# Kernel optimization log

Measured on AMD Instinct MI355X. Metric: run time of the kernel, lower is better.

## Reference

```python
import jax, jax.numpy as jnp
import numpy as np

N = 100_000      # nodes
E = 600_000      # edges (before self-loops)
F_IN = 128       # in_channels
H0, H1 = 64, 128 # hidden_channels
D = 512          # FLAGS.D
G = 512          # number of graphs in batch
OUT = 1          # FLAGS.out_dim


def _lin(key, fan_in, fan_out):
    k1, k2 = jax.random.split(key)
    s = 1.0 / np.sqrt(fan_in)
    return (jax.random.uniform(k1, (fan_in, fan_out), jnp.float32, -s, s),
            jax.random.uniform(k2, (fan_out,), jnp.float32, -s, s))


def setup_inputs() -> dict:
    key = jax.random.key(0)
    ks = jax.random.split(key, 12)
    x = jax.random.normal(ks[0], (N, F_IN), jnp.float32)
    src = jax.random.randint(ks[1], (E,), 0, N, jnp.int32)
    dst = jax.random.randint(ks[2], (E,), 0, N, jnp.int32)
    batch = jnp.sort(jax.random.randint(ks[3], (N,), 0, G, jnp.int32))
    Wc0, bc0 = _lin(ks[4], F_IN, H0)   # GCNConv 1
    Wc1, bc1 = _lin(ks[5], H0, H1)     # GCNConv 2
    Wf, bf = _lin(ks[6], H1, D)        # first_MLP: Linear(128, D)
    Wh0, bh0 = _lin(ks[7], D, D // 2)  # MLP head hidden layers
    Wh1, bh1 = _lin(ks[8], D // 2, D // 4)
    Wh2, bh2 = _lin(ks[9], D // 4, D // 8)
    Wo, bo = _lin(ks[10], D // 8, OUT) # MLP head output
    return dict(x=x, src=src, dst=dst, batch=batch,
                Wc0=Wc0, bc0=bc0, Wc1=Wc1, bc1=bc1, Wf=Wf, bf=bf,
                Wh0=Wh0, bh0=bh0, Wh1=Wh1, bh1=bh1, Wh2=Wh2, bh2=bh2,
                Wo=Wo, bo=bo)


def gcn_conv(x, src, dst, W, b):
    """PyG GCNConv: add self-loops, sym-normalized neighbor sum, then bias."""
    n = x.shape[0]
    loop = jnp.arange(n, dtype=src.dtype)
    s = jnp.concatenate([src, loop])
    d = jnp.concatenate([dst, loop])
    deg = jax.ops.segment_sum(jnp.ones(s.shape[0], x.dtype), d, num_segments=n)
    dinv = jnp.where(deg > 0, jax.lax.rsqrt(deg), 0.0)
    h = x @ W                                  # [n, out]
    coeff = (dinv[s] * dinv[d])[:, None]       # [e+n, 1]
    out = jax.ops.segment_sum(h[s] * coeff, d, num_segments=n)
    return out + b


def reference(x, src, dst, batch, Wc0, bc0, Wc1, bc1, Wf, bf,
              Wh0, bh0, Wh1, bh1, Wh2, bh2, Wo, bo):
    # two GCNConv layers + ReLU (dropout p=0.0 is a no-op)
    h = jax.nn.relu(gcn_conv(x, src, dst, Wc0, bc0))
    h = jax.nn.relu(gcn_conv(h, src, dst, Wc1, bc1))
    # global mean pool over graphs
    cnt = jax.ops.segment_sum(jnp.ones(h.shape[0], h.dtype), batch, num_segments=G)
    g = jax.ops.segment_sum(h, batch, num_segments=G) / jnp.maximum(cnt, 1.0)[:, None]
    # first_MLP (plain Linear) then MLP head with ReLU hidden layers
    e = g @ Wf + bf
    e = jax.nn.relu(e @ Wh0 + bh0)
    e = jax.nn.relu(e @ Wh1 + bh1)
    e = jax.nn.relu(e @ Wh2 + bh2)
    out = e @ Wo + bo
    return out
```

## Files before the change

### kernel.cpp

```cpp
#include <hip/hip_runtime.h>
#include <hip/hip_bf16.h>

#define NN   100000
#define NE   600000
#define FIN  128
#define H0   64
#define H1   128
#define NG   512
#define BM   64
#define XP   132
#define AP   68

__global__ void hist_kernel(const int* __restrict__ idx, int* __restrict__ cnt, int n)
{
    int i = blockIdx.x * blockDim.x + threadIdx.x;
    int stride = gridDim.x * blockDim.x;
    for (; i < n; i += stride) atomicAdd(&cnt[idx[i]], 1);
}

__global__ void batch_count_kernel(const int* __restrict__ batch,
                                   int* __restrict__ cnt, int n)
{
    const int g = blockIdx.x * blockDim.x + threadIdx.x;
    if (g >= NG) return;
    int lo = 0, hi = n;
    while (lo < hi) { const int m = (lo + hi) >> 1; if (batch[m] < g) lo = m + 1; else hi = m; }
    const int start = lo;
    lo = 0; hi = n;
    while (lo < hi) { const int m = (lo + hi) >> 1; if (batch[m] < g + 1) lo = m + 1; else hi = m; }
    cnt[g] = lo - start;
}

__global__ void dinv_kernel(const int* __restrict__ deg, float* __restrict__ dinv, int n)
{
    int i = blockIdx.x * blockDim.x + threadIdx.x;
    if (i < n) dinv[i] = 1.0f / sqrtf((float)(deg[i] + 1));
}

__global__ __launch_bounds__(256) void scan1_kernel(
    const int* __restrict__ deg, int* __restrict__ rp, int* __restrict__ bsum, int n)
{
    __shared__ int tmp[256];
    const int t = threadIdx.x;
    const int i = blockIdx.x * 256 + t;
    int v = (i < n) ? deg[i] : 0;
    tmp[t] = v;
    __syncthreads();
    #pragma unroll
    for (int off = 1; off < 256; off <<= 1) {
        int a = (t >= off) ? tmp[t - off] : 0;
        __syncthreads();
        tmp[t] += a;
        __syncthreads();
    }
    if (i < n) rp[i] = tmp[t] - v;
    if (t == 255) bsum[blockIdx.x] = tmp[255];
}

__global__ __launch_bounds__(512) void scan2_kernel(
    const int* __restrict__ bsum, int* __restrict__ boff, int nb)
{
    __shared__ int tmp[512];
    const int t = threadIdx.x;
    int v = (t < nb) ? bsum[t] : 0;
    tmp[t] = v;
    __syncthreads();
    #pragma unroll
    for (int off = 1; off < 512; off <<= 1) {
        int a = (t >= off) ? tmp[t - off] : 0;
        __syncthreads();
        tmp[t] += a;
        __syncthreads();
    }
    if (t < nb) boff[t] = tmp[t] - v;
}

__global__ __launch_bounds__(256) void scan3_kernel(
    int* __restrict__ rp, int* __restrict__ wcur, const int* __restrict__ boff, int n)
{
    const int i = blockIdx.x * 256 + threadIdx.x;
    if (i < n) {
        const int v = rp[i] + boff[blockIdx.x];
        rp[i] = v;
        wcur[i] = v;
    }
}

__global__ void fill_kernel(const int* __restrict__ src, const int* __restrict__ dst,
                            int* __restrict__ wcur, int* __restrict__ csr, int ne)
{
    int i = blockIdx.x * blockDim.x + threadIdx.x;
    const int stride = gridDim.x * blockDim.x;
    for (; i < ne; i += stride) {
        const int d = dst[i];
        const int p = atomicAdd(&wcur[d], 1);
        csr[p] = src[i];
    }
}

__global__ __launch_bounds__(256) void gemm1_kernel(
    const float* __restrict__ x, const float* __restrict__ W,
    const float* __restrict__ dinv, float* __restrict__ h0s, int n)
{
    __shared__ float Wl[FIN * H0];
    __shared__ float xs[BM * XP];
    const int t = threadIdx.x;
    for (int i = t; i < FIN * H0 / 4; i += 256)
        ((float4*)Wl)[i] = ((const float4*)W)[i];

    const int lane = t & 63;
    const int w    = t >> 6;
    const int rsub = lane >> 4;
    const int j0   = (lane & 15) * 4;
    const int wrow = w * 16 + rsub * 4;
    const int ntiles = (n + BM - 1) / BM;

    for (int tile = blockIdx.x; tile < ntiles; tile += gridDim.x) {
        const int row0  = tile * BM;
        const int nrows = min(BM, n - row0);
        __syncthreads();
        {
            const float4* xg = (const float4*)(x + (size_t)row0 * FIN);
            const int nf4 = nrows * (FIN / 4);
            for (int idx = t; idx < nf4; idx += 256) {
                const int r  = idx >> 5;
                const int c4 = idx & 31;
                *(float4*)&xs[r * XP + (c4 << 2)] = xg[idx];
            }
        }
        __syncthreads();

        float acc[4][4] = {};
        const float* xr = xs + wrow * XP;
        #pragma unroll 4
        for (int k = 0; k < FIN; k += 4) {
            const float4 w0 = *(const float4*)&Wl[(k + 0) * H0 + j0];
            const float4 w1 = *(const float4*)&Wl[(k + 1) * H0 + j0];
            const float4 w2 = *(const float4*)&Wl[(k + 2) * H0 + j0];
            const float4 w3 = *(const float4*)&Wl[(k + 3) * H0 + j0];
            #pragma unroll
            for (int r = 0; r < 4; ++r) {
                const float4 xv = *(const float4*)&xr[r * XP + k];
                acc[r][0] += xv.x * w0.x; acc[r][0] += xv.y * w1.x;
                acc[r][0] += xv.z * w2.x; acc[r][0] += xv.w * w3.x;
                acc[r][1] += xv.x * w0.y; acc[r][1] += xv.y * w1.y;
                acc[r][1] += xv.z * w2.y; acc[r][1] += xv.w * w3.y;
                acc[r][2] += xv.x * w0.z; acc[r][2] += xv.y * w1.z;
                acc[r][2] += xv.z * w2.z; acc[r][2] += xv.w * w3.z;
                acc[r][3] += xv.x * w0.w; acc[r][3] += xv.y * w1.w;
                acc[r][3] += xv.z * w2.w; acc[r][3] += xv.w * w3.w;
            }
        }
        #pragma unroll
        for (int r = 0; r < 4; ++r) {
            const int row = row0 + wrow + r;
            if (row < n) {
                const float dv = dinv[row];
                float4 o;
                o.x = acc[r][0] * dv; o.y = acc[r][1] * dv;
                o.z = acc[r][2] * dv; o.w = acc[r][3] * dv;
                *(float4*)&h0s[(size_t)row * H0 + j0] = o;
            }
        }
    }
}

template <int MODE>
__global__ __launch_bounds__(256) void gather_kernel(
    const float* __restrict__ hin, const int* __restrict__ rowptr,
    const int* __restrict__ deg, const int* __restrict__ csr,
    const float* __restrict__ dinv, const float* __restrict__ bias,
    float* __restrict__ hout, int n)
{
    const int lane = threadIdx.x & 63;
    int wid = (blockIdx.x * blockDim.x + threadIdx.x) >> 6;
    const int nw = (gridDim.x * blockDim.x) >> 6;
    for (int d = wid; d < n; d += nw) {
        const int r0  = rowptr[d];
        const int cnt = deg[d];
        float acc = hin[(size_t)d * H0 + lane];
        int k = 0;
        for (; k + 1 < cnt; k += 2) {
            const int s0 = csr[r0 + k];
            const int s1 = csr[r0 + k + 1];
            acc += hin[(size_t)s0 * H0 + lane];
            acc += hin[(size_t)s1 * H0 + lane];
        }
        if (k < cnt) acc += hin[(size_t)csr[r0 + k] * H0 + lane];
        const float dv = dinv[d];
        if (MODE == 0)
            hout[(size_t)d * H0 + lane] = fmaxf(acc * dv + bias[lane], 0.f) * dv;
        else
            hout[(size_t)d * H0 + lane] = acc * dv;
    }
}

__global__ __launch_bounds__(256) void gemm2_pool_kernel(
    const float* __restrict__ a , const float* __restrict__ W ,
    const float* __restrict__ bc1, const int* __restrict__ batch,
    float* __restrict__ gsum, int n)
{
    __shared__ float Wl[H0 * H1];
    __shared__ float as[BM * AP];
    __shared__ float red[4][H1];
    __shared__ int   bs[BM];
    const int t = threadIdx.x;
    for (int i = t; i < H0 * H1 / 4; i += 256)
        ((float4*)Wl)[i] = ((const float4*)W)[i];

    const int lane = t & 63;
    const int w    = t >> 6;
    const int rsub = lane >> 4;
    const int cA   = (lane & 15) * 4;
    const int cB   = cA + 64;
    const int wrow = w * 16 + rsub * 4;
    const float4 bA = *(const float4*)&bc1[cA];
    const float4 bB = *(const float4*)&bc1[cB];
    const int ntiles = (n + BM - 1) / BM;

    for (int tile = blockIdx.x; tile < ntiles; tile += gridDim.x) {
        const int row0  = tile * BM;
        const int nrows = min(BM, n - row0);
        __syncthreads();
        {
            const float4* ag = (const float4*)(a + (size_t)row0 * H0);
            const int nf4 = nrows * (H0 / 4);
            for (int idx = t; idx < nf4; idx += 256) {
                const int r  = idx >> 4;
                const int c4 = idx & 15;
                *(float4*)&as[r * AP + (c4 << 2)] = ag[idx];
            }
            if (t < nrows) bs[t] = batch[row0 + t];
        }
        __syncthreads();

        float acc[4][8] = {};
        const float* ar = as + wrow * AP;
        #pragma unroll 4
        for (int k = 0; k < H0; k += 4) {
            float4 wa[4], wb[4];
            #pragma unroll
            for (int kk = 0; kk < 4; ++kk) {
                wa[kk] = *(const float4*)&Wl[(k + kk) * H1 + cA];
                wb[kk] = *(const float4*)&Wl[(k + kk) * H1 + cB];
            }
            #pragma unroll
            for (int r = 0; r < 4; ++r) {
                const float4 xv = *(const float4*)&ar[r * AP + k];
                acc[r][0] += xv.x * wa[0].x; acc[r][0] += xv.y * wa[1].x;
                acc[r][0] += xv.z * wa[2].x; acc[r][0] += xv.w * wa[3].x;
                acc[r][1] += xv.x * wa[0].y; acc[r][1] += xv.y * wa[1].y;
                acc[r][1] += xv.z * wa[2].y; acc[r][1] += xv.w * wa[3].y;
                acc[r][2] += xv.x * wa[0].z; acc[r][2] += xv.y * wa[1].z;
                acc[r][2] += xv.z * wa[2].z; acc[r][2] += xv.w * wa[3].z;
                acc[r][3] += xv.x * wa[0].w; acc[r][3] += xv.y * wa[1].w;
                acc[r][3] += xv.z * wa[2].w; acc[r][3] += xv.w * wa[3].w;
                acc[r][4] += xv.x * wb[0].x; acc[r][4] += xv.y * wb[1].x;
                acc[r][4] += xv.z * wb[2].x; acc[r][4] += xv.w * wb[3].x;
                acc[r][5] += xv.x * wb[0].y; acc[r][5] += xv.y * wb[1].y;
                acc[r][5] += xv.z * wb[2].y; acc[r][5] += xv.w * wb[3].y;
                acc[r][6] += xv.x * wb[0].z; acc[r][6] += xv.y * wb[1].z;
                acc[r][6] += xv.z * wb[2].z; acc[r][6] += xv.w * wb[3].z;
                acc[r][7] += xv.x * wb[0].w; acc[r][7] += xv.y * wb[1].w;
                acc[r][7] += xv.z * wb[2].w; acc[r][7] += xv.w * wb[3].w;
            }
        }

        const float bv[8] = {bA.x, bA.y, bA.z, bA.w, bB.x, bB.y, bB.z, bB.w};
        const bool uni = (nrows == BM) && (bs[0] == bs[BM - 1]);
        if (uni) {
            float s[8];
            #pragma unroll
            for (int c = 0; c < 8; ++c) {
                s[c] = fmaxf(acc[0][c] + bv[c], 0.f) + fmaxf(acc[1][c] + bv[c], 0.f)
                     + fmaxf(acc[2][c] + bv[c], 0.f) + fmaxf(acc[3][c] + bv[c], 0.f);
                s[c] += __shfl_xor(s[c], 16);
                s[c] += __shfl_xor(s[c], 32);
            }
            if (rsub == 0) {
                #pragma unroll
                for (int c = 0; c < 4; ++c) red[w][cA + c] = s[c];
                #pragma unroll
                for (int c = 0; c < 4; ++c) red[w][cB + c] = s[c + 4];
            }
            __syncthreads();
            if (t < H1)
                atomicAdd(&gsum[(size_t)bs[0] * H1 + t],
                          red[0][t] + red[1][t] + red[2][t] + red[3][t]);
        } else {
            int gcur = -1; float run[8];
            #pragma unroll
            for (int r = 0; r < 4; ++r) {
                const int row = wrow + r;
                if (row < nrows) {
                    const int g = bs[row];
                    if (g != gcur) {
                        if (gcur >= 0) {
                            #pragma unroll
                            for (int c = 0; c < 4; ++c)
                                atomicAdd(&gsum[(size_t)gcur * H1 + cA + c], run[c]);
                            #pragma unroll
                            for (int c = 0; c < 4; ++c)
                                atomicAdd(&gsum[(size_t)gcur * H1 + cB + c], run[c + 4]);
                        }
                        gcur = g;
                        #pragma unroll
                        for (int c = 0; c < 8; ++c) run[c] = fmaxf(acc[r][c] + bv[c], 0.f);
                    } else {
                        #pragma unroll
                        for (int c = 0; c < 8; ++c) run[c] += fmaxf(acc[r][c] + bv[c], 0.f);
                    }
                }
            }
            if (gcur >= 0) {
                #pragma unroll
                for (int c = 0; c < 4; ++c)
                    atomicAdd(&gsum[(size_t)gcur * H1 + cA + c], run[c]);
                #pragma unroll
                for (int c = 0; c < 4; ++c)
                    atomicAdd(&gsum[(size_t)gcur * H1 + cB + c], run[c + 4]);
            }
        }
    }
}

__global__ __launch_bounds__(256) void mlp_kernel(
    const float* __restrict__ gsum, const int* __restrict__ cnt,
    const float* __restrict__ Wf,  const float* __restrict__ bf,
    const float* __restrict__ Wh0, const float* __restrict__ bh0,
    const float* __restrict__ Wh1, const float* __restrict__ bh1,
    const float* __restrict__ Wh2, const float* __restrict__ bh2,
    const float* __restrict__ Wo,  const float* __restrict__ bo,
    float* __restrict__ out)
{
    __shared__ float gm[128];
    __shared__ float e0[512];
    __shared__ float e1[256];
    __shared__ float e2[128];
    __shared__ float e3[64];
    const int gi = blockIdx.x;
    const int t  = threadIdx.x;

    if (t < 128) {
        const int c = cnt[gi];
        gm[t] = gsum[gi * 128 + t] * (1.0f / (float)max(c, 1));
    }
    __syncthreads();

    for (int jj = t; jj < 512; jj += 256) {
        float acc = bf[jj];
        for (int k = 0; k < 128; ++k) acc += gm[k] * Wf[k * 512 + jj];
        e0[jj] = acc;
    }
    __syncthreads();

    {
        float acc = bh0[t];
        for (int k = 0; k < 512; ++k) acc += e0[k] * Wh0[k * 256 + t];
        if (t < 256) e1[t] = fmaxf(acc, 0.f);
    }
    __syncthreads();

    if (t < 128) {
        float acc = bh1[t];
        for (int k = 0; k < 256; ++k) acc += e1[k] * Wh1[k * 128 + t];
        e2[t] = fmaxf(acc, 0.f);
    }
    __syncthreads();

    if (t < 64) {
        float acc = bh2[t];
        for (int k = 0; k < 128; ++k) acc += e2[k] * Wh2[k * 64 + t];
        e3[t] = fmaxf(acc, 0.f);
    }
    __syncthreads();

    if (t < 64) {
        float p = e3[t] * Wo[t];
        #pragma unroll
        for (int off = 32; off > 0; off >>= 1) p += __shfl_down(p, off);
        if (t == 0) out[gi] = p + bo[0];
    }
}

extern "C" void kernel_launch(void* const* d_in, const int* in_sizes, int n_in,
                              void* d_out, int out_size, void* d_ws, size_t ws_size,
                              hipStream_t stream)
{
    const float* x    = (const float*)d_in[0];
    const int*   src  = (const int*)  d_in[1];
    const int*   dst  = (const int*)  d_in[2];
    const int*   batch= (const int*)  d_in[3];
    const float* Wc0  = (const float*)d_in[4];
    const float* bc0  = (const float*)d_in[5];
    const float* Wc1  = (const float*)d_in[6];
    const float* bc1  = (const float*)d_in[7];
    const float* Wf   = (const float*)d_in[8];
    const float* bf   = (const float*)d_in[9];
    const float* Wh0  = (const float*)d_in[10];
    const float* bh0  = (const float*)d_in[11];
    const float* Wh1  = (const float*)d_in[12];
    const float* bh1  = (const float*)d_in[13];
    const float* Wh2  = (const float*)d_in[14];
    const float* bh2  = (const float*)d_in[15];
    const float* Wo   = (const float*)d_in[16];
    const float* bo   = (const float*)d_in[17];
    float* out = (float*)d_out;

    const int n = NN, ne = NE;
    const int nblk = (n + 255) / 256;
    const int ntiles = (n + BM - 1) / BM;

    char* ws = (char*)d_ws;
    size_t off = 0;
    auto alloc = [&](size_t bytes) {
        void* p = ws + off;
        off = (off + bytes + 255) & ~(size_t)255;
        return p;
    };
    int*   deg    = (int*)  alloc((size_t)n * 4);
    float* dinv   = (float*)alloc((size_t)n * 4);
    int*   rowptr = (int*)  alloc((size_t)n * 4);
    int*   wcur   = (int*)  alloc((size_t)n * 4);
    int*   bsum   = (int*)  alloc(512 * 4);
    int*   boff   = (int*)  alloc(512 * 4);
    int*   csr    = (int*)  alloc((size_t)ne * 4);
    float* h0s    = (float*)alloc((size_t)n * H0 * 4);
    float* h1s    = (float*)alloc((size_t)n * H0 * 4);
    float* agg1   = (float*)alloc((size_t)n * H0 * 4);
    float* gsum   = (float*)alloc((size_t)NG * H1 * 4);
    int*   cnt    = (int*)  alloc((size_t)NG * 4);

    hipMemsetAsync(deg,  0, (size_t)n * 4, stream);
    hipMemsetAsync(gsum, 0, (size_t)NG * H1 * 4, stream);

    hist_kernel<<<1024, 256, 0, stream>>>(dst, deg, ne);
    batch_count_kernel<<<2, 256, 0, stream>>>(batch, cnt, n);
    dinv_kernel<<<nblk, 256, 0, stream>>>(deg, dinv, n);

    scan1_kernel<<<nblk, 256, 0, stream>>>(deg, rowptr, bsum, n);
    scan2_kernel<<<1, 512, 0, stream>>>(bsum, boff, nblk);
    scan3_kernel<<<nblk, 256, 0, stream>>>(rowptr, wcur, boff, n);
    fill_kernel<<<1024, 256, 0, stream>>>(src, dst, wcur, csr, ne);

    gemm1_kernel<<<ntiles, 256, 0, stream>>>(x, Wc0, dinv, h0s, n);
    gather_kernel<0><<<4096, 256, 0, stream>>>(h0s, rowptr, deg, csr, dinv, bc0, h1s, n);

    gather_kernel<1><<<4096, 256, 0, stream>>>(h1s, rowptr, deg, csr, dinv, bc0, agg1, n);
    gemm2_pool_kernel<<<ntiles, 256, 0, stream>>>(agg1, Wc1, bc1, batch, gsum, n);

    mlp_kernel<<<NG, 256, 0, stream>>>(gsum, cnt, Wf, bf, Wh0, bh0,
                                       Wh1, bh1, Wh2, bh2, Wo, bo, out);
}
```

Measured before the change: 389.1 us.

## Read GEMM weights from global/L1 instead of LDS; wave-cooperative CSR index loads in gather

Both GEMM kernels stop staging the weight matrix in shared memory and read it directly from global memory, relying on cache. This frees LDS and adds a launch-bounds occupancy hint of 4 blocks. The gather kernel now has the wave load up to 64 neighbor indices in one coalesced read and broadcast them with shuffles, unrolled by four. The trade-off is that weight reads now go through the cache path instead of LDS, which may add latency in the inner GEMM loop.

```diff
diff --git a/kernel.cpp b/kernel.cpp
--- a/kernel.cpp
+++ b/kernel.cpp
@@ -98,16 +98,12 @@
     }
 }
 
-__global__ __launch_bounds__(256) void gemm1_kernel(
+__global__ __launch_bounds__(256, 4) void gemm1_kernel(
     const float* __restrict__ x, const float* __restrict__ W,
     const float* __restrict__ dinv, float* __restrict__ h0s, int n)
 {
-    __shared__ float Wl[FIN * H0];
     __shared__ float xs[BM * XP];
     const int t = threadIdx.x;
-    for (int i = t; i < FIN * H0 / 4; i += 256)
-        ((float4*)Wl)[i] = ((const float4*)W)[i];
-
     const int lane = t & 63;
     const int w    = t >> 6;
     const int rsub = lane >> 4;
@@ -134,10 +130,10 @@
         const float* xr = xs + wrow * XP;
         #pragma unroll 4
         for (int k = 0; k < FIN; k += 4) {
-            const float4 w0 = *(const float4*)&Wl[(k + 0) * H0 + j0];
-            const float4 w1 = *(const float4*)&Wl[(k + 1) * H0 + j0];
-            const float4 w2 = *(const float4*)&Wl[(k + 2) * H0 + j0];
-            const float4 w3 = *(const float4*)&Wl[(k + 3) * H0 + j0];
+            const float4 w0 = *(const float4*)&W[(k + 0) * H0 + j0];
+            const float4 w1 = *(const float4*)&W[(k + 1) * H0 + j0];
+            const float4 w2 = *(const float4*)&W[(k + 2) * H0 + j0];
+            const float4 w3 = *(const float4*)&W[(k + 3) * H0 + j0];
             #pragma unroll
             for (int r = 0; r < 4; ++r) {
                 const float4 xv = *(const float4*)&xr[r * XP + k];
@@ -179,14 +175,26 @@
         const int r0  = rowptr[d];
         const int cnt = deg[d];
         float acc = hin[(size_t)d * H0 + lane];
-        int k = 0;
-        for (; k + 1 < cnt; k += 2) {
-            const int s0 = csr[r0 + k];
-            const int s1 = csr[r0 + k + 1];
-            acc += hin[(size_t)s0 * H0 + lane];
-            acc += hin[(size_t)s1 * H0 + lane];
-        }
-        if (k < cnt) acc += hin[(size_t)csr[r0 + k] * H0 + lane];
+        for (int base = 0; base < cnt; base += 64) {
+            const int m = min(64, cnt - base);
+            const int sv = (lane < m) ? csr[r0 + base + lane] : 0;
+            int k = 0;
+            for (; k + 3 < m; k += 4) {
+                const int s0 = __shfl(sv, k);
+                const int s1 = __shfl(sv, k + 1);
+                const int s2 = __shfl(sv, k + 2);
+                const int s3 = __shfl(sv, k + 3);
+                const float v0 = hin[(size_t)s0 * H0 + lane];
+                const float v1 = hin[(size_t)s1 * H0 + lane];
+                const float v2 = hin[(size_t)s2 * H0 + lane];
+                const float v3 = hin[(size_t)s3 * H0 + lane];
+                acc += v0; acc += v1; acc += v2; acc += v3;
+            }
+            for (; k < m; ++k) {
+                const int s = __shfl(sv, k);
+                acc += hin[(size_t)s * H0 + lane];
+            }
+        }
         const float dv = dinv[d];
         if (MODE == 0)
             hout[(size_t)d * H0 + lane] = fmaxf(acc * dv + bias[lane], 0.f) * dv;
@@ -195,19 +203,15 @@
     }
 }
 
-__global__ __launch_bounds__(256) void gemm2_pool_kernel(
+__global__ __launch_bounds__(256, 4) void gemm2_pool_kernel(
     const float* __restrict__ a , const float* __restrict__ W ,
     const float* __restrict__ bc1, const int* __restrict__ batch,
     float* __restrict__ gsum, int n)
 {
-    __shared__ float Wl[H0 * H1];
     __shared__ float as[BM * AP];
     __shared__ float red[4][H1];
     __shared__ int   bs[BM];
     const int t = threadIdx.x;
-    for (int i = t; i < H0 * H1 / 4; i += 256)
-        ((float4*)Wl)[i] = ((const float4*)W)[i];
-
     const int lane = t & 63;
     const int w    = t >> 6;
     const int rsub = lane >> 4;
@@ -241,8 +245,8 @@
             float4 wa[4], wb[4];
             #pragma unroll
             for (int kk = 0; kk < 4; ++kk) {
-                wa[kk] = *(const float4*)&Wl[(k + kk) * H1 + cA];
-                wb[kk] = *(const float4*)&Wl[(k + kk) * H1 + cB];
+                wa[kk] = *(const float4*)&W[(k + kk) * H1 + cA];
+                wb[kk] = *(const float4*)&W[(k + kk) * H1 + cB];
             }
             #pragma unroll
             for (int r = 0; r < 4; ++r) {
```

Measured after the change: 432.8 us. 1.11x slower.
